# Kernel optimization log

Measured on AMD Instinct MI355X. Metric: run time of the kernel, lower is better.

## Reference

```python
import jax, jax.numpy as jnp
import numpy as np

CUTOFF = 5.0
NB, NA, NEIGH, NTYPE, NWAVE = 32, 1024, 64, 4, 16
P = NA * NEIGH  # pairs per batch


def setup_inputs() -> dict:
    key = jax.random.key(0)
    ks = jax.random.split(key, 8)
    coordinates = jax.random.normal(ks[0], (NB, NA, 3), dtype=jnp.float32)
    shifts = jax.random.normal(ks[1], (NB, P, 3), dtype=jnp.float32)  # all > -1e9 -> no padding
    rs = jax.random.uniform(ks[2], (NTYPE, NWAVE), jnp.float32, 0.0, CUTOFF)
    inta = jax.random.uniform(ks[3], (NTYPE, NWAVE), jnp.float32, 0.1, 1.0)
    params = jax.random.normal(ks[4], (NTYPE,), dtype=jnp.float32)  # unused in forward, kept for parity
    numatoms = jax.random.randint(ks[5], (NB, 1), 0, NA, dtype=jnp.int32)  # unused in forward
    atom_index = jax.random.randint(ks[6], (NB, 2, P), 0, NA, dtype=jnp.int32)
    species = jax.random.randint(ks[7], (NB * NA,), 0, NTYPE, dtype=jnp.int32)
    return {"coordinates": coordinates, "shifts": shifts, "rs": rs, "inta": inta,
            "params": params, "numatoms": numatoms, "atom_index": atom_index, "species": species}


def reference(coordinates, shifts, rs, inta, params, numatoms, atom_index, species):
    nb, na = coordinates.shape[:2]
    ntype, nwave = rs.shape
    totnatom = nb * na
    coords = coordinates.reshape(totnatom, 3)
    # (nb, 2, P) -> (2, nb*P) with per-batch global offsets (b * na)
    ai = jnp.transpose(atom_index, (1, 0, 2)).reshape(2, -1)
    offs = jnp.repeat(jnp.arange(nb, dtype=ai.dtype) * na, atom_index.shape[2])
    idx12 = ai + offs[None, :]
    sh = shifts.reshape(-1, 3)
    valid = jnp.all(sh > -1e9, axis=-1)  # padding mask (all valid for these inputs)
    # gather neighbor coordinates, displacement, distance
    dist_vec = coords[idx12[0]] - coords[idx12[1]] + sh
    distances = jnp.linalg.norm(dist_vec, axis=-1)  # (npairs,)
    spec = species[idx12[0]]  # (npairs,) atom type of center atom
    # type-gathered gaussian radial basis: exp(-10*inta_t*(r - rs_t)^2)
    radial = jnp.exp(-10.0 * inta[spec] * jnp.square(distances[:, None] - rs[spec]))  # (npairs, nwave)
    # cosine cutoff: 0.5*(cos(pi*min(r/rc,1))+1)
    fc = 0.5 * (jnp.cos(jnp.pi * jnp.minimum(distances / CUTOFF, 1.0)) + 1.0)
    orbital = radial * (fc * valid.astype(radial.dtype))[:, None]  # (npairs, nwave)
    # per-(atom, type) scatter-add, then square
    dens = jnp.zeros((totnatom, ntype, nwave), dtype=coordinates.dtype)
    dens = dens.at[idx12[0], spec].add(orbital)
    return jnp.square(dens).reshape(totnatom, ntype * nwave)
```

## Files before the change

kernel.cpp:

```cpp
#include <hip/hip_runtime.h>
#include <math.h>

#define NB     32
#define NA     1024
#define NTYPE  4
#define NWAVE  16
#define PPB    65536
#define NPAIRS (NB * PPB)
#define TOTATOM (NB * NA)
#define DENS_ELEMS (TOTATOM * NTYPE * NWAVE)
#define CUTOFF      5.0f
#define CUTOFF_INV  0.2f
#define PI_F 3.14159265358979323846f

#define NSPLIT 8
#define BLOCK_A 1024
#define PPBLK (PPB / NSPLIT)
#define KITERS_A (PPBLK / BLOCK_A)
#define NSEG (NB * NSPLIT)
#define ENC_SCALE (65535.0f / CUTOFF)
#define DEC_SCALE (CUTOFF / 65535.0f)
#define FC_ENC 65535.0f
#define FC_DEC (1.0f / 65535.0f)

#define CSR_BYTES  ((size_t)NSEG * PPBLK * 4)
#define OFFS_U32S  ((size_t)NSEG * (NA + 1))
#define WS2_NEEDED (CSR_BYTES + OFFS_U32S * 4)

#define GBLOCK 256
#define APB    32
#define SLAB_CAP 2432

typedef __attribute__((address_space(3))) unsigned lds_u32;
__device__ __forceinline__ unsigned lds_uinc(unsigned* p) {
    lds_u32* lp = (lds_u32*)(unsigned)(unsigned long long)p;
    return __atomic_fetch_add(lp, 1u, __ATOMIC_RELAXED);
}

__global__ __launch_bounds__(BLOCK_A) void radial_bin_csr(
    const float* __restrict__ coords,
    const float* __restrict__ shifts,
    const int*   __restrict__ atom_index,
    unsigned*    __restrict__ csr,
    unsigned*    __restrict__ offs)
{
    __shared__ unsigned hist[NA];
    __shared__ unsigned base[NA + 1];
    __shared__ unsigned wsum[16];
    __shared__ unsigned scsr[PPBLK];

    const int b    = blockIdx.x >> 3;
    const int s    = blockIdx.x & (NSPLIT - 1);
    const int seg  = b * NSPLIT + s;
    const int tid  = threadIdx.x;
    const int lane = tid & 63;
    const int wid  = tid >> 6;

    hist[tid] = 0u;
    __syncthreads();

    const int* ai0 = atom_index + (b * 2 + 0) * PPB + s * PPBLK;
    const int* ai1 = atom_index + (b * 2 + 1) * PPB + s * PPBLK;
    const float* cb  = coords + (size_t)b * NA * 3;
    const float* shb = shifts + ((size_t)b * PPB + s * PPBLK) * 3;

    int      ik[KITERS_A];
    unsigned rk[KITERS_A];
    unsigned ek[KITERS_A];

    #pragma unroll
    for (int k = 0; k < KITERS_A; ++k) {
        const int pp = k * BLOCK_A + tid;
        const int i = ai0[pp];
        const int j = ai1[pp];

        const float sx = shb[pp * 3 + 0];
        const float sy = shb[pp * 3 + 1];
        const float sz = shb[pp * 3 + 2];
        const bool valid = (sx > -1e9f) && (sy > -1e9f) && (sz > -1e9f);

        const float dx = cb[i * 3 + 0] - cb[j * 3 + 0] + sx;
        const float dy = cb[i * 3 + 1] - cb[j * 3 + 1] + sy;
        const float dz = cb[i * 3 + 2] - cb[j * 3 + 2] + sz;
        const float r  = sqrtf(dx * dx + dy * dy + dz * dz);

        if (valid && r < CUTOFF) {
            const unsigned rank = lds_uinc(&hist[i]);
            unsigned e = (unsigned)(r * ENC_SCALE + 0.5f);
            if (e > 65535u) e = 65535u;
            const float fc = 0.5f * (__cosf(r * (PI_F * CUTOFF_INV)) + 1.0f);
            unsigned fq = (unsigned)(fc * FC_ENC + 0.5f);
            if (fq > 65535u) fq = 65535u;
            ik[k] = i;
            rk[k] = rank;
            ek[k] = (fq << 16) | e;
        } else {
            ik[k] = -1;
            rk[k] = 0u;
            ek[k] = 0u;
        }
    }
    __syncthreads();

    const unsigned h = hist[tid];
    unsigned x = h;
    #pragma unroll
    for (int d = 1; d < 64; d <<= 1) {
        const unsigned v = __shfl_up(x, d);
        if (lane >= d) x += v;
    }
    if (lane == 63) wsum[wid] = x;
    __syncthreads();
    if (tid < 16) {
        const unsigned own = wsum[tid];
        unsigned y = own;
        #pragma unroll
        for (int d = 1; d < 16; d <<= 1) {
            const unsigned v = __shfl_up(y, d);
            if (lane >= d) y += v;
        }
        wsum[tid] = y - own;
    }
    __syncthreads();
    const unsigned incl = x + wsum[wid];
    base[tid] = incl - h;
    if (tid == BLOCK_A - 1) base[NA] = incl;
    __syncthreads();

    #pragma unroll
    for (int k = 0; k < KITERS_A; ++k) {
        if (ik[k] >= 0) {
            scsr[base[ik[k]] + rk[k]] = ek[k];
        }
    }
    __syncthreads();

    {
        const uint4* src = reinterpret_cast<const uint4*>(scsr);
        uint4* dst = reinterpret_cast<uint4*>(csr + (size_t)seg * PPBLK);
        #pragma unroll
        for (int k = 0; k < PPBLK / 4 / BLOCK_A; ++k)
            dst[k * BLOCK_A + tid] = src[k * BLOCK_A + tid];
    }
    unsigned* og = offs + (size_t)seg * (NA + 1);
    og[tid] = base[tid];
    if (tid == 0) og[NA] = base[NA];
}

__global__ __launch_bounds__(GBLOCK) void radial_gather_slab(
    const unsigned* __restrict__ csr,
    const unsigned* __restrict__ offs,
    const float* __restrict__ rs,
    const float* __restrict__ inta,
    const int*   __restrict__ species,
    float*       __restrict__ out)
{
    __shared__ unsigned slab[SLAB_CAP];
    __shared__ unsigned sofs[NSPLIT][APB + 1];
    __shared__ unsigned runbase[NSPLIT];

    const int tid = threadIdx.x;
    const int g0  = blockIdx.x * APB;
    const int b   = g0 >> 10;
    const int a0  = g0 & (NA - 1);

    for (int idx = tid; idx < NSPLIT * (APB + 1); idx += GBLOCK) {
        const int s = idx / (APB + 1);
        const int a = idx - s * (APB + 1);
        sofs[s][a] = offs[(size_t)(b * NSPLIT + s) * (NA + 1) + a0 + a];
    }
    __syncthreads();

    if (tid == 0) {
        unsigned acc = 0;
        #pragma unroll
        for (int s = 0; s < NSPLIT; ++s) {
            runbase[s] = acc;
            acc += sofs[s][APB] - sofs[s][0];
        }
    }
    __syncthreads();

    {
        const int s = tid >> 5;
        const int l = tid & 31;
        const unsigned lo  = sofs[s][0];
        const unsigned len = sofs[s][APB] - lo;
        const unsigned* src = csr + (size_t)(b * NSPLIT + s) * PPBLK + lo;
        const unsigned bse = runbase[s];
        for (unsigned k = l; k < len; k += 32) {
            const unsigned p = bse + k;
            if (p < SLAB_CAP) slab[p] = src[k];
        }
    }
    __syncthreads();

    const int at = tid >> 3;
    const int w0 = (tid & 7) << 1;
    const int g  = g0 + at;
    const int spec = species[g];

    const float rs0 = rs[(spec << 4) + w0];
    const float rs1 = rs[(spec << 4) + w0 + 1];
    const float ia0 = -10.0f * inta[(spec << 4) + w0];
    const float ia1 = -10.0f * inta[(spec << 4) + w0 + 1];

    float acc0 = 0.0f, acc1 = 0.0f;
    #pragma unroll
    for (int s = 0; s < NSPLIT; ++s) {
        const unsigned off0 = sofs[s][0];
        unsigned lo = runbase[s] + (sofs[s][at]     - off0);
        unsigned hi = runbase[s] + (sofs[s][at + 1] - off0);
        if (hi > SLAB_CAP) hi = SLAB_CAP;
        if (lo > hi) lo = hi;
        for (unsigned k = lo; k < hi; ++k) {
            const unsigned v = slab[k];
            const float r   = (float)(v & 0xFFFFu) * DEC_SCALE;
            const float fcv = (float)(v >> 16) * FC_DEC;
            const float d0 = r - rs0;
            const float d1 = r - rs1;
            acc0 = fmaf(fcv, __expf(ia0 * d0 * d0), acc0);
            acc1 = fmaf(fcv, __expf(ia1 * d1 * d1), acc1);
        }
    }

    const float2 sq = make_float2(acc0 * acc0, acc1 * acc1);
    const float2 zero = make_float2(0.f, 0.f);
    float* orow = out + (size_t)g * (NTYPE * NWAVE) + w0;
    #pragma unroll
    for (int ty = 0; ty < NTYPE; ++ty)
        *reinterpret_cast<float2*>(orow + ty * NWAVE) = (ty == spec) ? sq : zero;
}

__global__ __launch_bounds__(256) void radial_pair_atomic(
    const float* __restrict__ coords, const float* __restrict__ shifts,
    const float* __restrict__ rs, const float* __restrict__ inta,
    const int* __restrict__ atom_index, const int* __restrict__ species,
    float* __restrict__ dens)
{
    int p = blockIdx.x * blockDim.x + threadIdx.x;
    if (p >= NPAIRS) return;
    int b  = p >> 16;
    int pp = p & (PPB - 1);
    int i = atom_index[(b * 2 + 0) * PPB + pp] + b * NA;
    int j = atom_index[(b * 2 + 1) * PPB + pp] + b * NA;
    float sx = shifts[p * 3 + 0], sy = shifts[p * 3 + 1], sz = shifts[p * 3 + 2];
    bool valid = (sx > -1e9f) && (sy > -1e9f) && (sz > -1e9f);
    float dx = coords[i * 3 + 0] - coords[j * 3 + 0] + sx;
    float dy = coords[i * 3 + 1] - coords[j * 3 + 1] + sy;
    float dz = coords[i * 3 + 2] - coords[j * 3 + 2] + sz;
    float r  = sqrtf(dx * dx + dy * dy + dz * dz);
    int spec = species[i];
    float x  = fminf(r * CUTOFF_INV, 1.0f);
    float fc = 0.5f * (__cosf(x * PI_F) + 1.0f);
    if (!valid) fc = 0.0f;
    const float* rsrow   = rs   + spec * NWAVE;
    const float* intarow = inta + spec * NWAVE;
    float* dst = dens + ((size_t)i * NTYPE + spec) * NWAVE;
    #pragma unroll
    for (int w = 0; w < NWAVE; ++w) {
        float d   = r - rsrow[w];
        float val = fc * __expf(-10.0f * intarow[w] * d * d);
        atomicAdd(dst + w, val);
    }
}

__global__ __launch_bounds__(256) void square_kernel(float* __restrict__ out)
{
    int i = blockIdx.x * blockDim.x + threadIdx.x;
    if (i * 4 >= DENS_ELEMS) return;
    float4* p = reinterpret_cast<float4*>(out) + i;
    float4 v = *p;
    v.x *= v.x; v.y *= v.y; v.z *= v.z; v.w *= v.w;
    *p = v;
}

extern "C" void kernel_launch(void* const* d_in, const int* in_sizes, int n_in,
                              void* d_out, int out_size, void* d_ws, size_t ws_size,
                              hipStream_t stream) {
    const float* coords     = (const float*)d_in[0];
    const float* shifts     = (const float*)d_in[1];
    const float* rs         = (const float*)d_in[2];
    const float* inta       = (const float*)d_in[3];
    const int*   atom_index = (const int*)d_in[6];
    const int*   species    = (const int*)d_in[7];
    float* out = (float*)d_out;

    if (ws_size >= WS2_NEEDED) {
        unsigned* csr  = (unsigned*)d_ws;
        unsigned* offs = (unsigned*)((char*)d_ws + CSR_BYTES);

        radial_bin_csr<<<dim3(NSEG), dim3(BLOCK_A), 0, stream>>>(
            coords, shifts, atom_index, csr, offs);
        radial_gather_slab<<<dim3(TOTATOM / APB), dim3(GBLOCK), 0, stream>>>(
            csr, offs, rs, inta, species, out);
    } else {
        hipMemsetAsync(d_out, 0, (size_t)DENS_ELEMS * sizeof(float), stream);
        radial_pair_atomic<<<dim3((NPAIRS + 255) / 256), dim3(256), 0, stream>>>(
            coords, shifts, rs, inta, atom_index, species, out);
        square_kernel<<<dim3((DENS_ELEMS / 4 + 255) / 256), dim3(256), 0, stream>>>(out);
    }
}
```

Measured before the change: 38.29 us.

## Repack slab into per-atom contiguous decoded float2 list and use exp2

The gather kernel now builds a per-atom concatenated list of decoded (r, fc) float2 values in shared memory. It uses two warp-shuffle prefix scans, one across the 8 splits and one across the 32 atoms. The inner loop then becomes one contiguous loop per atom instead of 8 segmented loops, and it reads pre-decoded floats. The exponential is also switched to the native exp2 with LOG2E folded into the coefficient. The cost is an extra repack pass, serial per-thread copy loops, more shared memory and additional barriers.

Result: faster. 34.61 us (-9.6%).

```diff
diff --git a/kernel.cpp b/kernel.cpp
--- a/kernel.cpp
+++ b/kernel.cpp
@@ -12,6 +12,7 @@
 #define CUTOFF      5.0f
 #define CUTOFF_INV  0.2f
 #define PI_F 3.14159265358979323846f
+#define LOG2E 1.4426950408889634f
 
 #define NSPLIT 8
 #define BLOCK_A 1024
@@ -147,7 +148,7 @@
     if (tid == 0) og[NA] = base[NA];
 }
 
-__global__ __launch_bounds__(GBLOCK) void radial_gather_slab(
+__global__ __launch_bounds__(GBLOCK) void radial_gather_repack(
     const unsigned* __restrict__ csr,
     const unsigned* __restrict__ offs,
     const float* __restrict__ rs,
@@ -156,8 +157,11 @@
     float*       __restrict__ out)
 {
     __shared__ unsigned slab[SLAB_CAP];
+    __shared__ float2   concat[SLAB_CAP];
     __shared__ unsigned sofs[NSPLIT][APB + 1];
     __shared__ unsigned runbase[NSPLIT];
+    __shared__ unsigned tots[APB];
+    __shared__ unsigned atomCat[APB + 1];
 
     const int tid = threadIdx.x;
     const int g0  = blockIdx.x * APB;
@@ -179,6 +183,17 @@
             acc += sofs[s][APB] - sofs[s][0];
         }
     }
+    const int rat = tid >> 3;
+    const int rs8 = tid & 7;
+    const unsigned cnt = sofs[rs8][rat + 1] - sofs[rs8][rat];
+    unsigned xin = cnt;
+    #pragma unroll
+    for (int d = 1; d < 8; d <<= 1) {
+        const unsigned v = __shfl_up(xin, d, 8);
+        if (rs8 >= d) xin += v;
+    }
+    const unsigned segPfx = xin - cnt;
+    if (rs8 == 7) tots[rat] = xin;
     __syncthreads();
 
     {
@@ -195,6 +210,34 @@
     }
     __syncthreads();
 
+    if (tid < 32) {
+        const unsigned t = tots[tid];
+        unsigned x = t;
+        #pragma unroll
+        for (int d = 1; d < 32; d <<= 1) {
+            const unsigned v = __shfl_up(x, d, 32);
+            if (tid >= d) x += v;
+        }
+        atomCat[tid] = x - t;
+        if (tid == 31) atomCat[32] = x;
+    }
+    __syncthreads();
+
+    {
+        const unsigned src0 = runbase[rs8] + (sofs[rs8][rat] - sofs[rs8][0]);
+        const unsigned dst0 = atomCat[rat] + segPfx;
+        for (unsigned k = 0; k < cnt; ++k) {
+            const unsigned sp = src0 + k;
+            const unsigned dp = dst0 + k;
+            if (sp < SLAB_CAP && dp < SLAB_CAP) {
+                const unsigned v = slab[sp];
+                concat[dp] = make_float2((float)(v & 0xFFFFu) * DEC_SCALE,
+                                         (float)(v >> 16) * FC_DEC);
+            }
+        }
+    }
+    __syncthreads();
+
     const int at = tid >> 3;
     const int w0 = (tid & 7) << 1;
     const int g  = g0 + at;
@@ -202,26 +245,20 @@
 
     const float rs0 = rs[(spec << 4) + w0];
     const float rs1 = rs[(spec << 4) + w0 + 1];
-    const float ia0 = -10.0f * inta[(spec << 4) + w0];
-    const float ia1 = -10.0f * inta[(spec << 4) + w0 + 1];
+    const float ia0 = -10.0f * LOG2E * inta[(spec << 4) + w0];
+    const float ia1 = -10.0f * LOG2E * inta[(spec << 4) + w0 + 1];
+
+    const unsigned lo = atomCat[at];
+    unsigned hi = atomCat[at + 1];
+    if (hi > SLAB_CAP) hi = SLAB_CAP;
 
     float acc0 = 0.0f, acc1 = 0.0f;
-    #pragma unroll
-    for (int s = 0; s < NSPLIT; ++s) {
-        const unsigned off0 = sofs[s][0];
-        unsigned lo = runbase[s] + (sofs[s][at]     - off0);
-        unsigned hi = runbase[s] + (sofs[s][at + 1] - off0);
-        if (hi > SLAB_CAP) hi = SLAB_CAP;
-        if (lo > hi) lo = hi;
-        for (unsigned k = lo; k < hi; ++k) {
-            const unsigned v = slab[k];
-            const float r   = (float)(v & 0xFFFFu) * DEC_SCALE;
-            const float fcv = (float)(v >> 16) * FC_DEC;
-            const float d0 = r - rs0;
-            const float d1 = r - rs1;
-            acc0 = fmaf(fcv, __expf(ia0 * d0 * d0), acc0);
-            acc1 = fmaf(fcv, __expf(ia1 * d1 * d1), acc1);
-        }
+    for (unsigned k = lo; k < hi; ++k) {
+        const float2 e = concat[k];
+        const float d0 = e.x - rs0;
+        const float d1 = e.x - rs1;
+        acc0 = fmaf(e.y, __builtin_amdgcn_exp2f(ia0 * d0 * d0), acc0);
+        acc1 = fmaf(e.y, __builtin_amdgcn_exp2f(ia1 * d1 * d1), acc1);
     }
 
     const float2 sq = make_float2(acc0 * acc0, acc1 * acc1);
@@ -292,7 +329,7 @@
 
         radial_bin_csr<<<dim3(NSEG), dim3(BLOCK_A), 0, stream>>>(
             coords, shifts, atom_index, csr, offs);
-        radial_gather_slab<<<dim3(TOTATOM / APB), dim3(GBLOCK), 0, stream>>>(
+        radial_gather_repack<<<dim3(TOTATOM / APB), dim3(GBLOCK), 0, stream>>>(
             csr, offs, rs, inta, species, out);
     } else {
         hipMemsetAsync(d_out, 0, (size_t)DENS_ELEMS * sizeof(float), stream);
```
